# Optimization experiments

Measured on AMD Instinct MI355X. Metric: run time of the kernel, lower is better.

Reference implementation:

```python
import jax, jax.numpy as jnp
import numpy as np

N, C = 1000000, 64
K = 64


def setup_inputs() -> dict:
    key = jax.random.key(0)
    k1, k2 = jax.random.split(key)
    point_feat = jax.random.normal(k1, (N, C), dtype=jnp.float32)
    # points in [-1, 1)^3 so floor indices land in [0, K)
    points = jax.random.uniform(k2, (N, 3), dtype=jnp.float32) * 2.0 - 1.0
    return {"point_feat": point_feat, "points": points, "k": K}


def reference(point_feat, points, k):
    # voxel index per point: floor((p+1)*k/2) dot [k^2, k, 1]
    p = (points + 1.0) * (k / 2.0)
    pi = jnp.floor(p).astype(jnp.int32)
    pi = jnp.clip(pi, 0, k - 1)  # guard exact boundary p == 1.0
    ks = jnp.array([k * k, k, 1], dtype=jnp.int32)
    pidx = pi @ ks  # (N,) flat cell index in [0, k^3)
    num_cells = k ** 3
    # scatter-mean: sum features per cell, divide by per-cell point count
    sums = jax.ops.segment_sum(point_feat, pidx, num_segments=num_cells)  # (k^3, C)
    counts = jax.ops.segment_sum(jnp.ones((pidx.shape[0],), dtype=point_feat.dtype),
                                 pidx, num_segments=num_cells)  # (k^3,)
    denom = jnp.where(counts > 0, counts, 1.0)
    out = sums / denom[:, None]
    return out.reshape((k, k, k, point_feat.shape[1]))
```

## Files before the change

### kernel.cpp

```cpp
#include <hip/hip_runtime.h>


#define KGRID  64
#define NCH    64
#define NCELLS (KGRID * KGRID * KGRID)
#define CAP    16
#define SPILLCAP 8192

__device__ __forceinline__ int cell_of(float px, float py, float pz) {
    int ix = min(max((int)floorf((px + 1.0f) * 32.0f), 0), KGRID - 1);
    int iy = min(max((int)floorf((py + 1.0f) * 32.0f), 0), KGRID - 1);
    int iz = min(max((int)floorf((pz + 1.0f) * 32.0f), 0), KGRID - 1);
    return (ix << 12) | (iy << 6) | iz;
}

__device__ __forceinline__ void fadd4(float4& a, const float4& b) {
    a.x += b.x; a.y += b.y; a.z += b.z; a.w += b.w;
}

__global__ __launch_bounds__(256) void assign_pts(
    const float* __restrict__ pts,
    int* __restrict__ counts,
    int* __restrict__ nspill,
    int* __restrict__ spill,
    int* __restrict__ bucket,
    int n)
{
    int t = blockIdx.x * blockDim.x + threadIdx.x;
    int p0 = t * 4;
    if (p0 >= n) return;
    if (p0 + 4 <= n) {
        const float4* p4 = (const float4*)(pts + (size_t)p0 * 3);
        float4 a = p4[0], b = p4[1], c = p4[2];
        int cid[4];
        cid[0] = cell_of(a.x, a.y, a.z);
        cid[1] = cell_of(a.w, b.x, b.y);
        cid[2] = cell_of(b.z, b.w, c.x);
        cid[3] = cell_of(c.y, c.z, c.w);
        #pragma unroll
        for (int i = 0; i < 4; ++i) {
            int slot = atomicAdd(&counts[cid[i]], 1);
            if (slot < CAP) {
                bucket[(size_t)cid[i] * CAP + slot] = p0 + i;
            } else {
                int s = atomicAdd(nspill, 1);
                if (s < SPILLCAP) { spill[2 * s] = cid[i]; spill[2 * s + 1] = p0 + i; }
            }
        }
    } else {
        for (int p = p0; p < n; ++p) {
            int c = cell_of(pts[3 * p], pts[3 * p + 1], pts[3 * p + 2]);
            int slot = atomicAdd(&counts[c], 1);
            if (slot < CAP) {
                bucket[(size_t)c * CAP + slot] = p;
            } else {
                int s = atomicAdd(nspill, 1);
                if (s < SPILLCAP) { spill[2 * s] = c; spill[2 * s + 1] = p; }
            }
        }
    }
}

__global__ __launch_bounds__(256) void reduce_bucket(
    const float4* __restrict__ feat4,
    const int* __restrict__ counts,
    const int* __restrict__ nspill,
    const int* __restrict__ spill,
    const int* __restrict__ bucket,
    float4* __restrict__ out4)
{
    int lane = threadIdx.x & 63;
    int wave = (int)((blockIdx.x * blockDim.x + threadIdx.x) >> 6);
    int grp  = lane >> 4;
    int ch4  = lane & 15;
    int cell = wave * 4 + grp;

    int cnt = counts[cell];
    const int4* bk = (const int4*)(bucket + (size_t)cell * CAP);
    int4 q0 = bk[0];
    int4 q1 = bk[1];

    float4 acc = make_float4(0.f, 0.f, 0.f, 0.f);
    if (cnt > 0) {
        int len = min(cnt, CAP);
        int e0 = q0.x;
        int e1 = (len > 1) ? q0.y : e0;
        int e2 = (len > 2) ? q0.z : e0;
        int e3 = (len > 3) ? q0.w : e0;
        int e4 = (len > 4) ? q1.x : e0;
        int e5 = (len > 5) ? q1.y : e0;
        int e6 = (len > 6) ? q1.z : e0;
        int e7 = (len > 7) ? q1.w : e0;
        const float4* fb = feat4 + ch4;
        float4 f0 = fb[(size_t)e0 * 16];
        float4 f1 = fb[(size_t)e1 * 16];
        float4 f2 = fb[(size_t)e2 * 16];
        float4 f3 = fb[(size_t)e3 * 16];
        float4 f4 = fb[(size_t)e4 * 16];
        float4 f5 = fb[(size_t)e5 * 16];
        float4 f6 = fb[(size_t)e6 * 16];
        float4 f7 = fb[(size_t)e7 * 16];
        acc = f0;
        if (len > 1) fadd4(acc, f1);
        if (len > 2) fadd4(acc, f2);
        if (len > 3) fadd4(acc, f3);
        if (len > 4) fadd4(acc, f4);
        if (len > 5) fadd4(acc, f5);
        if (len > 6) fadd4(acc, f6);
        if (len > 7) fadd4(acc, f7);
        if (len > 8) {
            for (int i = 8; i < len; ++i) {
                int p = bucket[(size_t)cell * CAP + i];
                fadd4(acc, fb[(size_t)p * 16]);
            }
        }
        if (cnt > CAP) {
            int ns = min(*nspill, SPILLCAP);
            for (int s = 0; s < ns; ++s) {
                if (spill[2 * s] == cell) fadd4(acc, fb[(size_t)spill[2 * s + 1] * 16]);
            }
        }
        float inv = 1.0f / (float)cnt;
        acc.x *= inv; acc.y *= inv; acc.z *= inv; acc.w *= inv;
    }
    out4[(size_t)wave * 64 + lane] = acc;
}

extern "C" void kernel_launch(void* const* d_in, const int* in_sizes, int n_in,
                              void* d_out, int out_size, void* d_ws, size_t ws_size,
                              hipStream_t stream)
{
    const float* feat = (const float*)d_in[0];
    const float* pts  = (const float*)d_in[1];
    float* out = (float*)d_out;

    const int n = in_sizes[0] / NCH;

    int* counts = (int*)d_ws;
    int* nspill = counts + NCELLS;
    int* spill  = nspill + 4;
    int* bucket = spill + 2 * SPILLCAP;

    hipMemsetAsync(counts, 0, (size_t)(NCELLS + 4) * sizeof(int), stream);

    int t4 = (n + 3) / 4;
    int pblocks = (t4 + 255) / 256;
    assign_pts<<<pblocks, 256, 0, stream>>>(pts, counts, nspill, spill, bucket, n);

    reduce_bucket<<<NCELLS / 16, 256, 0, stream>>>(
        (const float4*)feat, counts, nspill, spill, bucket, (float4*)out);
}
```

Baseline: 450.4 us.

## Interleave per-cell count and point bucket into one 64-byte record

Per-cell counters and bucket slots now share one 16-int record: the count sits in slot 0 and up to 15 point indices follow, so CAP drops to 15. The atomic increment and the index store in assign_pts hit the same cache line, and reduce_bucket reads count and indices with four int4 loads from one line. The reduce kernel also drops the cnt>0 branch and uses a max(cnt,1) divisor instead. In exchange the workspace memset grows from about 1 MB to about 16 MB, and overflow past 15 points per cell goes to the slow spill path slightly more often.

```diff
diff --git a/kernel.cpp b/kernel.cpp
--- a/kernel.cpp
+++ b/kernel.cpp
@@ -4,7 +4,7 @@
 #define KGRID  64
 #define NCH    64
 #define NCELLS (KGRID * KGRID * KGRID)
-#define CAP    16
+#define CAP    15
 #define SPILLCAP 8192
 
 __device__ __forceinline__ int cell_of(float px, float py, float pz) {
@@ -20,10 +20,9 @@
 
 __global__ __launch_bounds__(256) void assign_pts(
     const float* __restrict__ pts,
-    int* __restrict__ counts,
+    int* __restrict__ rec,
     int* __restrict__ nspill,
     int* __restrict__ spill,
-    int* __restrict__ bucket,
     int n)
 {
     int t = blockIdx.x * blockDim.x + threadIdx.x;
@@ -39,9 +38,11 @@
         cid[3] = cell_of(c.y, c.z, c.w);
         #pragma unroll
         for (int i = 0; i < 4; ++i) {
-            int slot = atomicAdd(&counts[cid[i]], 1);
+            int* base = rec + ((size_t)cid[i] << 4);
+            int slot = __hip_atomic_fetch_add(base, 1, __ATOMIC_RELAXED,
+                                              __HIP_MEMORY_SCOPE_AGENT);
             if (slot < CAP) {
-                bucket[(size_t)cid[i] * CAP + slot] = p0 + i;
+                base[1 + slot] = p0 + i;
             } else {
                 int s = atomicAdd(nspill, 1);
                 if (s < SPILLCAP) { spill[2 * s] = cid[i]; spill[2 * s + 1] = p0 + i; }
@@ -50,9 +51,11 @@
     } else {
         for (int p = p0; p < n; ++p) {
             int c = cell_of(pts[3 * p], pts[3 * p + 1], pts[3 * p + 2]);
-            int slot = atomicAdd(&counts[c], 1);
+            int* base = rec + ((size_t)c << 4);
+            int slot = __hip_atomic_fetch_add(base, 1, __ATOMIC_RELAXED,
+                                              __HIP_MEMORY_SCOPE_AGENT);
             if (slot < CAP) {
-                bucket[(size_t)c * CAP + slot] = p;
+                base[1 + slot] = p;
             } else {
                 int s = atomicAdd(nspill, 1);
                 if (s < SPILLCAP) { spill[2 * s] = c; spill[2 * s + 1] = p; }
@@ -63,10 +66,9 @@
 
 __global__ __launch_bounds__(256) void reduce_bucket(
     const float4* __restrict__ feat4,
-    const int* __restrict__ counts,
+    const int* __restrict__ rec,
     const int* __restrict__ nspill,
     const int* __restrict__ spill,
-    const int* __restrict__ bucket,
     float4* __restrict__ out4)
 {
     int lane = threadIdx.x & 63;
@@ -75,54 +77,61 @@
     int ch4  = lane & 15;
     int cell = wave * 4 + grp;
 
-    int cnt = counts[cell];
-    const int4* bk = (const int4*)(bucket + (size_t)cell * CAP);
-    int4 q0 = bk[0];
-    int4 q1 = bk[1];
+    const int4* r4 = (const int4*)(rec + ((size_t)cell << 4));
+    int4 r0 = r4[0];
+    int4 r1 = r4[1];
+    int4 r2 = r4[2];
+    int4 r3 = r4[3];
+
+    int cnt = r0.x;
+    int len = min(cnt, CAP);
+    int e0 = (len > 0) ? r0.y : 0;
+    int e1 = (len > 1) ? r0.z : e0;
+    int e2 = (len > 2) ? r0.w : e0;
+    int e3 = (len > 3) ? r1.x : e0;
+    int e4 = (len > 4) ? r1.y : e0;
+    int e5 = (len > 5) ? r1.z : e0;
+    int e6 = (len > 6) ? r1.w : e0;
+    int e7 = (len > 7) ? r2.x : e0;
+
+    const float4* fb = feat4 + ch4;
+    float4 f0 = fb[(size_t)e0 * 16];
+    float4 f1 = fb[(size_t)e1 * 16];
+    float4 f2 = fb[(size_t)e2 * 16];
+    float4 f3 = fb[(size_t)e3 * 16];
+    float4 f4 = fb[(size_t)e4 * 16];
+    float4 f5 = fb[(size_t)e5 * 16];
+    float4 f6 = fb[(size_t)e6 * 16];
+    float4 f7 = fb[(size_t)e7 * 16];
 
     float4 acc = make_float4(0.f, 0.f, 0.f, 0.f);
-    if (cnt > 0) {
-        int len = min(cnt, CAP);
-        int e0 = q0.x;
-        int e1 = (len > 1) ? q0.y : e0;
-        int e2 = (len > 2) ? q0.z : e0;
-        int e3 = (len > 3) ? q0.w : e0;
-        int e4 = (len > 4) ? q1.x : e0;
-        int e5 = (len > 5) ? q1.y : e0;
-        int e6 = (len > 6) ? q1.z : e0;
-        int e7 = (len > 7) ? q1.w : e0;
-        const float4* fb = feat4 + ch4;
-        float4 f0 = fb[(size_t)e0 * 16];
-        float4 f1 = fb[(size_t)e1 * 16];
-        float4 f2 = fb[(size_t)e2 * 16];
-        float4 f3 = fb[(size_t)e3 * 16];
-        float4 f4 = fb[(size_t)e4 * 16];
-        float4 f5 = fb[(size_t)e5 * 16];
-        float4 f6 = fb[(size_t)e6 * 16];
-        float4 f7 = fb[(size_t)e7 * 16];
-        acc = f0;
-        if (len > 1) fadd4(acc, f1);
-        if (len > 2) fadd4(acc, f2);
-        if (len > 3) fadd4(acc, f3);
-        if (len > 4) fadd4(acc, f4);
-        if (len > 5) fadd4(acc, f5);
-        if (len > 6) fadd4(acc, f6);
-        if (len > 7) fadd4(acc, f7);
-        if (len > 8) {
-            for (int i = 8; i < len; ++i) {
-                int p = bucket[(size_t)cell * CAP + i];
-                fadd4(acc, fb[(size_t)p * 16]);
-            }
+    if (len > 0) fadd4(acc, f0);
+    if (len > 1) fadd4(acc, f1);
+    if (len > 2) fadd4(acc, f2);
+    if (len > 3) fadd4(acc, f3);
+    if (len > 4) fadd4(acc, f4);
+    if (len > 5) fadd4(acc, f5);
+    if (len > 6) fadd4(acc, f6);
+    if (len > 7) fadd4(acc, f7);
+
+    if (len > 8) {
+        fadd4(acc, fb[(size_t)r2.y * 16]);
+        if (len > 9)  fadd4(acc, fb[(size_t)r2.z * 16]);
+        if (len > 10) fadd4(acc, fb[(size_t)r2.w * 16]);
+        if (len > 11) fadd4(acc, fb[(size_t)r3.x * 16]);
+        if (len > 12) fadd4(acc, fb[(size_t)r3.y * 16]);
+        if (len > 13) fadd4(acc, fb[(size_t)r3.z * 16]);
+        if (len > 14) fadd4(acc, fb[(size_t)r3.w * 16]);
+    }
+    if (cnt > CAP) {
+        int ns = min(*nspill, SPILLCAP);
+        for (int s = 0; s < ns; ++s) {
+            if (spill[2 * s] == cell) fadd4(acc, fb[(size_t)spill[2 * s + 1] * 16]);
         }
-        if (cnt > CAP) {
-            int ns = min(*nspill, SPILLCAP);
-            for (int s = 0; s < ns; ++s) {
-                if (spill[2 * s] == cell) fadd4(acc, fb[(size_t)spill[2 * s + 1] * 16]);
-            }
-        }
-        float inv = 1.0f / (float)cnt;
-        acc.x *= inv; acc.y *= inv; acc.z *= inv; acc.w *= inv;
     }
+    float inv = 1.0f / (float)max(cnt, 1);
+    acc.x *= inv; acc.y *= inv; acc.z *= inv; acc.w *= inv;
+
     out4[(size_t)wave * 64 + lane] = acc;
 }
 
@@ -136,17 +145,16 @@
 
     const int n = in_sizes[0] / NCH;
 
-    int* counts = (int*)d_ws;
-    int* nspill = counts + NCELLS;
+    int* rec    = (int*)d_ws;
+    int* nspill = rec + (size_t)NCELLS * 16;
     int* spill  = nspill + 4;
-    int* bucket = spill + 2 * SPILLCAP;
 
-    hipMemsetAsync(counts, 0, (size_t)(NCELLS + 4) * sizeof(int), stream);
+    hipMemsetAsync(rec, 0, ((size_t)NCELLS * 16 + 4) * sizeof(int), stream);
 
     int t4 = (n + 3) / 4;
     int pblocks = (t4 + 255) / 256;
-    assign_pts<<<pblocks, 256, 0, stream>>>(pts, counts, nspill, spill, bucket, n);
+    assign_pts<<<pblocks, 256, 0, stream>>>(pts, rec, nspill, spill, n);
 
     reduce_bucket<<<NCELLS / 16, 256, 0, stream>>>(
-        (const float4*)feat, counts, nspill, spill, bucket, (float4*)out);
+        (const float4*)feat, rec, nspill, spill, (float4*)out);
 }
```

New measurement: 419.5 us. -6.9%, faster.
